# Kernel optimization log

Hardware: AMD Instinct MI355X
Metric: run time of the kernel (lower is better)

## Reference

```python
import jax, jax.numpy as jnp
import numpy as np

B, L_Q, S_KV, H, E = 4, 1024, 1024, 8, 64
IN_CH = OUT_CH = 512
MODES = 64
INDEX_Q = np.arange(MODES)   # 'lowest' mode selection -> range(0, modes)
INDEX_KV = np.arange(MODES)
SCALE = 1.0 / np.sqrt(OUT_CH)
FACTOR = 5


def setup_inputs() -> dict:
    key = jax.random.key(0)
    ks = jax.random.split(key, 7)
    tf_queries = jax.random.normal(ks[0], (B, L_Q, H, E), jnp.float32)
    queries = jax.random.normal(ks[1], (B, L_Q, H, E), jnp.float32)
    keys = jax.random.normal(ks[2], (B, S_KV, H, E), jnp.float32)
    values = jax.random.normal(ks[3], (B, S_KV, H, E), jnp.float32)
    mask = jnp.ones((1,), jnp.int32)  # unused by the module
    weights_fuse = jax.random.uniform(ks[4], (H, L_Q, 2), jnp.float32)
    # torch.rand with cfloat dtype samples re/im independently from U[0,1)
    w1_re = SCALE * jax.random.uniform(ks[5], (H, IN_CH // 8, OUT_CH // 8, MODES), jnp.float32)
    w1_im = SCALE * jax.random.uniform(ks[6], (H, IN_CH // 8, OUT_CH // 8, MODES), jnp.float32)
    return dict(tf_queries=tf_queries, queries=queries, keys=keys, values=values,
                mask=mask, weights_fuse=weights_fuse, w1_re=w1_re, w1_im=w1_im)


def get_sig_scores(n, queries, keys, scale, corr):
    # queries/keys: [B, L, H, E] (keys already aligned to L_Q)
    B_, Lq, H_, E_ = queries.shape
    Lk = keys.shape[1]
    q = jnp.transpose(queries, (0, 2, 1, 3))  # [B,H,L,E]
    k = jnp.transpose(keys, (0, 2, 1, 3))
    if corr:
        qf = jnp.fft.rfft(jnp.transpose(queries, (0, 2, 3, 1)), axis=-1)
        kf = jnp.fft.rfft(jnp.transpose(keys, (0, 2, 3, 1)), axis=-1)
        autocorr = jnp.transpose(jnp.fft.irfft(qf * jnp.conj(kf), axis=-1), (0, 1, 3, 2))  # [B,H,L,E]
    else:
        autocorr = q
    amp = jnp.linalg.norm(autocorr, axis=-1)           # [B,H,L]
    _, top_idx = jax.lax.top_k(amp, n)                 # [B,H,n]
    q_sel = jnp.take_along_axis(q, top_idx[..., None], axis=2)  # [B,H,n,E]
    scores = jnp.einsum('bhnd,bhmd->bhnm', q_sel, k) * scale    # [B,H,n,Lk]
    full = jnp.full((B_, H_, Lq, Lk), -jnp.inf, scores.dtype)
    bi = jnp.arange(B_)[:, None, None]
    hi = jnp.arange(H_)[None, :, None]
    full = full.at[bi, hi, top_idx].set(scores)        # scatter selected query rows
    # softmax over the query axis for every key position (transpose(2,3))
    return jax.nn.softmax(jnp.swapaxes(full, 2, 3), axis=-1)  # [B,H,Lk,Lq]


def reference(tf_queries, queries, keys, values, mask, weights_fuse, w1_re, w1_im):
    B_, Lq, H_, E_ = queries.shape
    S_ = keys.shape[1]
    xq = jnp.transpose(queries, (0, 2, 3, 1))  # [B,H,E,L_Q]
    xk = jnp.transpose(keys, (0, 2, 3, 1))     # [B,H,E,S]
    if Lq > S_:
        pad = jnp.zeros((B_, Lq - S_, H_, E_), keys.dtype)
        keys2 = jnp.concatenate([keys, pad], axis=1)
        values2 = jnp.concatenate([values, pad], axis=1)
    else:
        keys2 = keys[:, :Lq]
        values2 = values[:, :Lq]
    n_top = min(int(FACTOR * np.ceil(np.log(Lq))), Lq)

    attn_t = get_sig_scores(n_top, queries, keys2, SCALE, corr=True)
    attn_tf = get_sig_scores(n_top, tf_queries, keys2, SCALE, corr=False)

    nw = jax.nn.softmax(weights_fuse, axis=-1)  # [H,L_Q,2]
    fused = nw[None, :, :, 0, None] * attn_t + nw[None, :, :, 1, None] * attn_tf
    # dropout(p=0.1) in eval mode -> identity

    xq_ft = jnp.fft.rfft(xq, axis=-1)[:, :, :, INDEX_Q]   # [B,H,E,M]
    xk_ft = jnp.fft.rfft(xk, axis=-1)[:, :, :, INDEX_KV]  # [B,H,E,M]
    xqk = jnp.tanh(jnp.einsum('bhex,bhey->bhxy', xq_ft, xk_ft))  # complex tanh
    xqkv = jnp.einsum('bhxy,bhey->bhex', xqk, xk_ft)
    w1 = w1_re + 1j * w1_im
    xqkvw = jnp.einsum('bhex,heox->bhox', xqkv, w1)        # [B,H,O,M]
    out_ft = jnp.zeros((B_, H_, E_, Lq // 2 + 1), xqkvw.dtype)
    out_ft = out_ft.at[:, :, :, INDEX_Q].set(xqkvw)
    out = jnp.fft.irfft(out_ft / IN_CH / OUT_CH, n=Lq, axis=-1)  # [B,H,E,L_Q]

    output = jnp.einsum('bhlm,bhmd->bhld', fused, jnp.transpose(values2, (0, 2, 1, 3)))
    output = jnp.transpose(output, (0, 1, 3, 2))  # [B,H,D,L_Q]
    return (output + out) * 0.5
```

## Files before the change

kernel.cpp:

```cpp
#include <hip/hip_runtime.h>
#include <math.h>

#define B_ 4
#define H_ 8
#define L_ 1024
#define E_ 64
#define NTOP 35
#define SCALE_ 0.04419417382415922f


__device__ __forceinline__ void dev_stage(char* smem, int vbid,
                                          const float* __restrict__ q_g,
                                          const float* __restrict__ k_g,
                                          float* __restrict__ xtq,
                                          float* __restrict__ xtk) {
  float* tile = reinterpret_cast<float*>(smem);
  const int tc = vbid & 15;
  const int src = (vbid >> 4) & 1;
  const int bh = vbid >> 5;
  const int b = bh >> 3, h = bh & 7;
  const int t0 = tc * 64;
  const int tid = threadIdx.x;
  const float* in = src ? k_g : q_g;
  float* out = src ? xtk : xtq;

  for (int idx = tid; idx < 1024; idx += 256) {
    int t = idx >> 4, e4 = idx & 15;
    float4 v = reinterpret_cast<const float4*>(
        in + ((size_t)(b * L_ + t0 + t) * H_ + h) * E_)[e4];
    tile[t * 65 + e4 * 4 + 0] = v.x; tile[t * 65 + e4 * 4 + 1] = v.y;
    tile[t * 65 + e4 * 4 + 2] = v.z; tile[t * 65 + e4 * 4 + 3] = v.w;
  }
  __syncthreads();
  for (int idx = tid; idx < 1024; idx += 256) {
    int e = idx >> 4, t4 = idx & 15;
    float4 v = make_float4(tile[(t4 * 4 + 0) * 65 + e], tile[(t4 * 4 + 1) * 65 + e],
                           tile[(t4 * 4 + 2) * 65 + e], tile[(t4 * 4 + 3) * 65 + e]);
    reinterpret_cast<float4*>(out + ((size_t)(bh * 64 + e)) * 1024 + t0)[t4] = v;
  }
}

__device__ __forceinline__ void dev_tfqnorm(int vbid,
                                            const float* __restrict__ tfq,
                                            float* __restrict__ ampsum) {
  const int bh = vbid >> 2, qt = vbid & 3;
  const int b = bh >> 3, h = bh & 7;
  const int l = qt * 256 + threadIdx.x;
  const float4* p4 = reinterpret_cast<const float4*>(
      &tfq[((size_t)(b * L_ + l) * H_ + h) * E_]);
  float s = 0.f;
#pragma unroll
  for (int e4 = 0; e4 < 16; ++e4) {
    float4 v = p4[e4];
    s += v.x * v.x + v.y * v.y + v.z * v.z + v.w * v.w;
  }
  ampsum[(size_t)(bh * 2 + 1) * 1024 + l] = s;
}

__device__ __forceinline__ void dev_fft(char* smem, int vbid,
                                        const float* __restrict__ xtq,
                                        const float* __restrict__ xtk,
                                        float* __restrict__ amp2_part,
                                        float* __restrict__ qft,
                                        float* __restrict__ kft) {
  float* zre = reinterpret_cast<float*>(smem);
  float* zim = zre + 4096;
  float* ctab = zim + 4096;
  float* stab = ctab + 512;
  const int eg = vbid & 15;
  const int bh = vbid >> 4;
  const int tid = threadIdx.x;
  const float TWO_PI_N = 6.283185307179586f / 1024.0f;

  if (tid < 512) {
    float s, c;
    sincosf(TWO_PI_N * (float)tid, &s, &c);
    ctab[tid] = c; stab[tid] = s;
  }
  for (int idx = tid; idx < 1024; idx += 512) {
    int ee = idx >> 8, t4 = idx & 255;
    size_t ro = ((size_t)(bh * 64 + eg * 4 + ee)) * 1024;
    float4 qv = reinterpret_cast<const float4*>(xtq + ro)[t4];
    float4 kv = reinterpret_cast<const float4*>(xtk + ro)[t4];
    *reinterpret_cast<float4*>(&zre[ee * 1024 + t4 * 4]) = qv;
    *reinterpret_cast<float4*>(&zim[ee * 1024 + t4 * 4]) = kv;
  }
  __syncthreads();

  for (int s = 0; s < 10; ++s) {
    const int half = 512 >> s;
#pragma unroll
    for (int it = 0; it < 4; ++it) {
      int idx = tid + it * 512;
      int ee = idx >> 9;
      int bf = idx & 511;
      int j = bf & (half - 1);
      int p0 = ((bf >> (9 - s)) << (10 - s)) + j;
      int p1 = p0 + half;
      float ur = zre[ee * 1024 + p0], ui = zim[ee * 1024 + p0];
      float vr = zre[ee * 1024 + p1], vi = zim[ee * 1024 + p1];
      float dr = ur - vr, di = ui - vi;
      zre[ee * 1024 + p0] = ur + vr; zim[ee * 1024 + p0] = ui + vi;
      int twi = j << s;
      float c = ctab[twi], sn = stab[twi];
      zre[ee * 1024 + p1] = fmaf(dr, c, di * sn);
      zim[ee * 1024 + p1] = fmaf(di, c, -dr * sn);
    }
    __syncthreads();
  }

  float pr[8], pi_[8];
#pragma unroll
  for (int it = 0; it < 8; ++it) {
    int idx = tid + it * 512;
    int ee = idx >> 10;
    int p = idx & 1023;
    int m = __brev((unsigned)p) >> 22;
    int mp = (1024 - m) & 1023;
    int pp = __brev((unsigned)mp) >> 22;
    float ar = zre[ee * 1024 + p], ai = zim[ee * 1024 + p];
    float br = zre[ee * 1024 + pp], bi = zim[ee * 1024 + pp];
    float qr = 0.5f * (ar + br), qi = 0.5f * (ai - bi);
    float kr = 0.5f * (ai + bi), ki = -0.5f * (ar - br);
    pr[it]  = fmaf(qr, kr, qi * ki);
    pi_[it] = fmaf(qi, kr, -qr * ki);
    if (m < 64) {
      size_t o = ((size_t)(bh * 64 + eg * 4 + ee) * 64 + m) * 2;
      qft[o] = qr; qft[o + 1] = qi;
      kft[o] = kr; kft[o + 1] = ki;
    }
  }
  __syncthreads();
#pragma unroll
  for (int it = 0; it < 8; ++it) {
    int idx = tid + it * 512;
    int ee = idx >> 10;
    int p = idx & 1023;
    zre[ee * 1024 + p] = pr[it]; zim[ee * 1024 + p] = pi_[it];
  }
  __syncthreads();

  for (int idx = tid; idx < 2048; idx += 512) {
    int u = idx >> 10;
    int p = idx & 1023;
    int e0 = 2 * u, e1 = 2 * u + 1;
    float s_r = zre[e0 * 1024 + p] - zim[e1 * 1024 + p];
    float s_i = zim[e0 * 1024 + p] + zre[e1 * 1024 + p];
    zre[e0 * 1024 + p] = s_r; zim[e0 * 1024 + p] = s_i;
  }
  __syncthreads();

  for (int s = 9; s >= 0; --s) {
    const int half = 512 >> s;
#pragma unroll
    for (int it = 0; it < 2; ++it) {
      int idx = tid + it * 512;
      int ee = (idx >> 9) * 2;
      int bf = idx & 511;
      int j = bf & (half - 1);
      int p0 = ((bf >> (9 - s)) << (10 - s)) + j;
      int p1 = p0 + half;
      int twi = j << s;
      float c = ctab[twi], sn = stab[twi];
      float ur = zre[ee * 1024 + p0], ui = zim[ee * 1024 + p0];
      float wr = zre[ee * 1024 + p1], wi = zim[ee * 1024 + p1];
      float vr = fmaf(wr, c, -wi * sn);
      float vi = fmaf(wi, c, wr * sn);
      zre[ee * 1024 + p0] = ur + vr; zim[ee * 1024 + p0] = ui + vi;
      zre[ee * 1024 + p1] = ur - vr; zim[ee * 1024 + p1] = ui - vi;
    }
    __syncthreads();
  }

  for (int t = tid; t < 1024; t += 512) {
    float r0 = zre[t], i0 = zim[t];
    float r2 = zre[2 * 1024 + t], i2 = zim[2 * 1024 + t];
    amp2_part[(size_t)(bh * 16 + eg) * 1024 + t] =
        fmaf(r0, r0, fmaf(i0, i0, fmaf(r2, r2, i2 * i2)));
  }
}

__device__ __forceinline__ void dev_sel(char* smem, int vbid,
                                        const float* __restrict__ amp2_part,
                                        const float* __restrict__ ampsum,
                                        int* __restrict__ sel_ws) {
  float* amp = reinterpret_cast<float*>(smem);
  const int p = vbid;
  const int tid = threadIdx.x;

  if ((p & 1) == 0) {
    const int bh = p >> 1;
    for (int t = tid; t < 1024; t += 256) {
      float s = 0.f;
#pragma unroll
      for (int c = 0; c < 16; ++c)
        s += amp2_part[(size_t)(bh * 16 + c) * 1024 + t];
      amp[t] = s;
    }
  } else {
    for (int t = tid; t < 1024; t += 256)
      amp[t] = ampsum[(size_t)p * 1024 + t];
  }
  __syncthreads();

  if (tid < 64) {
    const int lane = tid;
    float val[16];
#pragma unroll
    for (int j = 0; j < 16; ++j) val[j] = amp[j * 64 + lane];

    float bv = -1.f; int bi = lane;
#pragma unroll
    for (int j = 0; j < 16; ++j) {
      if (val[j] > bv) { bv = val[j]; bi = j * 64 + lane; }
    }
    for (int it = 0; it < NTOP; ++it) {
      float v = bv; int i = bi;
#pragma unroll
      for (int d = 1; d < 64; d <<= 1) {
        float ov = __shfl_xor(v, d);
        int oi = __shfl_xor(i, d);
        if (ov > v || (ov == v && oi < i)) { v = ov; i = oi; }
      }
      if (lane == 0) sel_ws[p * 64 + it] = i;
      if ((i & 63) == lane) {
        int jr = i >> 6;
#pragma unroll
        for (int j = 0; j < 16; ++j) if (j == jr) val[j] = -1.f;
        bv = -1.f; bi = lane;
#pragma unroll
        for (int j = 0; j < 16; ++j) {
          if (val[j] > bv) { bv = val[j]; bi = j * 64 + lane; }
        }
      }
    }
  }
}

__device__ __forceinline__ void dev_attn(char* smem, int vbid,
                                         const float* __restrict__ q_g,
                                         const float* __restrict__ tfq,
                                         const float* __restrict__ k_g,
                                         const float* __restrict__ v_g,
                                         const float* __restrict__ wfuse,
                                         const int* __restrict__ sel_ws,
                                         float* __restrict__ out) {
  float4* qs4 = reinterpret_cast<float4*>(smem);
  float4* vs4 = qs4 + 2 * NTOP * 16;
  const int ac = vbid & 15;
  const int bh = vbid >> 4;
  const int b = bh >> 3, h = bh & 7;
  const int a0 = ac * 64;
  const int tid = threadIdx.x;

  for (int idx = tid; idx < 2 * NTOP * 16; idx += 256) {
    int src = idx / (NTOP * 16);
    int rem = idx - src * (NTOP * 16);
    int i = rem >> 4, e4 = rem & 15;
    int row = sel_ws[(bh * 2 + src) * 64 + i];
    size_t rb = ((size_t)(b * L_ + row) * H_ + h) * E_;
    const float* qbase = src ? tfq : q_g;
    qs4[(src * NTOP + i) * 16 + e4] = reinterpret_cast<const float4*>(qbase + rb)[e4];
    vs4[(src * NTOP + i) * 16 + e4] = reinterpret_cast<const float4*>(v_g + rb)[e4];
  }
  __syncthreads();

  const int qd = tid & 3, r = tid >> 2;
  const int a = a0 + r;
  const int eb = qd * 16;

  size_t krb = ((size_t)(b * L_ + a) * H_ + h) * E_;
  const float4* k4p = reinterpret_cast<const float4*>(k_g + krb);
  float4 kq[4];
#pragma unroll
  for (int j4 = 0; j4 < 4; ++j4) kq[j4] = k4p[qd * 4 + j4];

  float ct[NTOP], ctf[NTOP];
#pragma unroll
  for (int i = 0; i < NTOP; ++i) { ct[i] = 0.f; ctf[i] = 0.f; }

#pragma unroll
  for (int j4 = 0; j4 < 4; ++j4) {
    float4 kv = kq[j4];
#pragma unroll
    for (int i = 0; i < NTOP; ++i) {
      float4 q4 = qs4[(0 * NTOP + i) * 16 + qd * 4 + j4];
      ct[i] = fmaf(q4.x, kv.x, ct[i]); ct[i] = fmaf(q4.y, kv.y, ct[i]);
      ct[i] = fmaf(q4.z, kv.z, ct[i]); ct[i] = fmaf(q4.w, kv.w, ct[i]);
      float4 p4 = qs4[(1 * NTOP + i) * 16 + qd * 4 + j4];
      ctf[i] = fmaf(p4.x, kv.x, ctf[i]); ctf[i] = fmaf(p4.y, kv.y, ctf[i]);
      ctf[i] = fmaf(p4.z, kv.z, ctf[i]); ctf[i] = fmaf(p4.w, kv.w, ctf[i]);
    }
  }
#pragma unroll
  for (int i = 0; i < NTOP; ++i) {
    ct[i] += __shfl_xor(ct[i], 1);  ct[i] += __shfl_xor(ct[i], 2);
    ctf[i] += __shfl_xor(ctf[i], 1); ctf[i] += __shfl_xor(ctf[i], 2);
  }

  float wf0 = wfuse[(h * L_ + a) * 2 + 0];
  float wf1 = wfuse[(h * L_ + a) * 2 + 1];
  float wm = fmaxf(wf0, wf1);
  float ew0 = expf(wf0 - wm), ew1 = expf(wf1 - wm);
  float nw0 = ew0 / (ew0 + ew1), nw1 = ew1 / (ew0 + ew1);

  {
    float m = -1e30f;
#pragma unroll
    for (int i = 0; i < NTOP; ++i) { ct[i] *= SCALE_; m = fmaxf(m, ct[i]); }
    float sum = 0.f;
#pragma unroll
    for (int i = 0; i < NTOP; ++i) { ct[i] = expf(ct[i] - m); sum += ct[i]; }
    float c = 0.5f * nw0 / sum;
#pragma unroll
    for (int i = 0; i < NTOP; ++i) ct[i] *= c;
  }
  {
    float m = -1e30f;
#pragma unroll
    for (int i = 0; i < NTOP; ++i) { ctf[i] *= SCALE_; m = fmaxf(m, ctf[i]); }
    float sum = 0.f;
#pragma unroll
    for (int i = 0; i < NTOP; ++i) { ctf[i] = expf(ctf[i] - m); sum += ctf[i]; }
    float c = 0.5f * nw1 / sum;
#pragma unroll
    for (int i = 0; i < NTOP; ++i) ctf[i] *= c;
  }
#pragma unroll
  for (int j4 = 0; j4 < 4; ++j4) {
    float ax = 0.f, ay = 0.f, az = 0.f, aw = 0.f;
#pragma unroll
    for (int i = 0; i < NTOP; ++i) {
      float4 v4 = vs4[(0 * NTOP + i) * 16 + qd * 4 + j4];
      ax = fmaf(ct[i], v4.x, ax); ay = fmaf(ct[i], v4.y, ay);
      az = fmaf(ct[i], v4.z, az); aw = fmaf(ct[i], v4.w, aw);
    }
#pragma unroll
    for (int i = 0; i < NTOP; ++i) {
      float4 v4 = vs4[(1 * NTOP + i) * 16 + qd * 4 + j4];
      ax = fmaf(ctf[i], v4.x, ax); ay = fmaf(ctf[i], v4.y, ay);
      az = fmaf(ctf[i], v4.z, az); aw = fmaf(ctf[i], v4.w, aw);
    }
    int d = eb + j4 * 4;
    out[((size_t)(bh * 64 + d + 0)) * 1024 + a] = ax;
    out[((size_t)(bh * 64 + d + 1)) * 1024 + a] = ay;
    out[((size_t)(bh * 64 + d + 2)) * 1024 + a] = az;
    out[((size_t)(bh * 64 + d + 3)) * 1024 + a] = aw;
  }
}

__device__ __forceinline__ void dev_spec12(char* smem, int vbid,
                                           const float* __restrict__ qft,
                                           const float* __restrict__ kft,
                                           float* __restrict__ xre_g,
                                           float* __restrict__ xim_g) {
  float* kre = reinterpret_cast<float*>(smem);
  float* kim = kre + 4160;
  float* qre = kim + 4160;
  float* qim = qre + 512;
  float* tre = qim + 512;
  float* tim = tre + 512;
  const int xc = vbid & 7;
  const int bh = vbid >> 3;
  const int tid = threadIdx.x;

  for (int idx = tid; idx < 4096; idx += 256) {
    int e = idx >> 6, y = idx & 63;
    size_t o = ((size_t)(bh * 64 + e) * 64 + y) * 2;
    kre[e * 65 + y] = kft[o]; kim[e * 65 + y] = kft[o + 1];
  }
  for (int idx = tid; idx < 512; idx += 256) {
    int e = idx >> 3, xl = idx & 7;
    size_t o = ((size_t)(bh * 64 + e) * 64 + xc * 8 + xl) * 2;
    qre[e * 8 + xl] = qft[o]; qim[e * 8 + xl] = qft[o + 1];
  }
  __syncthreads();

  const int y = tid & 63, xg = tid >> 6;
#pragma unroll
  for (int xi = 0; xi < 2; ++xi) {
    int xl = xg + xi * 4;
    float ar = 0.f, ai = 0.f;
    for (int e = 0; e < 64; ++e) {
      float a = qre[e * 8 + xl], b = qim[e * 8 + xl];
      float c = kre[e * 65 + y], d = kim[e * 65 + y];
      ar = fmaf(a, c, fmaf(-b, d, ar));
      ai = fmaf(a, d, fmaf(b, c, ai));
    }
    float trv, tiv;
    float x2 = 2.f * ar, y2 = 2.f * ai;
    if (fabsf(x2) > 30.f) {
      trv = copysignf(1.f, ar); tiv = 0.f;
    } else {
      float sh = sinhf(x2), ch = coshf(x2);
      float sn = sinf(y2), cs = cosf(y2);
      float dd = ch + cs;
      trv = sh / dd; tiv = sn / dd;
    }
    tre[xl * 64 + y] = trv; tim[xl * 64 + y] = tiv;
  }
  __syncthreads();

  const int e2 = tid & 63, xg2 = tid >> 6;
#pragma unroll
  for (int xi = 0; xi < 2; ++xi) {
    int xl = xg2 + xi * 4;
    float ar = 0.f, ai = 0.f;
    for (int yy = 0; yy < 64; ++yy) {
      float a = tre[xl * 64 + yy], b = tim[xl * 64 + yy];
      float c = kre[e2 * 65 + yy], d = kim[e2 * 65 + yy];
      ar = fmaf(a, c, fmaf(-b, d, ar));
      ai = fmaf(a, d, fmaf(b, c, ai));
    }
    xre_g[(size_t)bh * 4096 + (xc * 8 + xl) * 64 + e2] = ar;
    xim_g[(size_t)bh * 4096 + (xc * 8 + xl) * 64 + e2] = ai;
  }
}

__device__ __forceinline__ void dev_w1(char* smem, int vbid,
                                       const float* __restrict__ xre_g,
                                       const float* __restrict__ xim_g,
                                       const float* __restrict__ w1re,
                                       const float* __restrict__ w1im,
                                       float* __restrict__ xw) {
  float* xre = reinterpret_cast<float*>(smem);
  float* xim = xre + 4160;
  float* redr = xim + 4160;
  float* redi = redr + 2048;
  const int oc = vbid & 7;
  const int bh = vbid >> 3;
  const int h = bh & 7;
  const int tid = threadIdx.x;

  for (int idx = tid; idx < 4096; idx += 256) {
    int x = idx >> 6, e = idx & 63;
    xre[e * 65 + x] = xre_g[(size_t)bh * 4096 + idx];
    xim[e * 65 + x] = xim_g[(size_t)bh * 4096 + idx];
  }
  __syncthreads();

  const int x = tid & 63, g = tid >> 6;
  float accr[8], acci[8];
#pragma unroll
  for (int oo = 0; oo < 8; ++oo) { accr[oo] = 0.f; acci[oo] = 0.f; }

  for (int ee = 0; ee < 16; ++ee) {
    int e = g * 16 + ee;
    float a = xre[e * 65 + x], b = xim[e * 65 + x];
    size_t wbase = (((size_t)h * 64 + e) * 64 + oc * 8) * 64 + x;
#pragma unroll
    for (int oo = 0; oo < 8; ++oo) {
      float c = w1re[wbase + (size_t)oo * 64];
      float d = w1im[wbase + (size_t)oo * 64];
      accr[oo] = fmaf(a, c, fmaf(-b, d, accr[oo]));
      acci[oo] = fmaf(a, d, fmaf(b, c, acci[oo]));
    }
  }
#pragma unroll
  for (int oo = 0; oo < 8; ++oo) {
    redr[g * 512 + oo * 64 + x] = accr[oo];
    redi[g * 512 + oo * 64 + x] = acci[oo];
  }
  __syncthreads();

  const float INV = 1.0f / (512.0f * 512.0f);
  for (int idx = tid; idx < 512; idx += 256) {
    int oo = idx >> 6, x2 = idx & 63;
    float r = redr[idx] + redr[512 + idx] + redr[1024 + idx] + redr[1536 + idx];
    float i = redi[idx] + redi[512 + idx] + redi[1024 + idx] + redi[1536 + idx];
    size_t oidx = ((size_t)(bh * 64 + oc * 8 + oo) * 64 + x2) * 2;
    xw[oidx] = r * INV;
    xw[oidx + 1] = i * INV;
  }
}

__device__ __forceinline__ void dev_final(char* smem, int vbid,
                                          const float* __restrict__ xw,
                                          float* __restrict__ out) {
  float* Xre = reinterpret_cast<float*>(smem);
  float* Xim = Xre + 512;
  const int tc = vbid & 3;
  const int oc = (vbid >> 2) & 7;
  const int bh = vbid >> 5;
  const int o0 = oc * 8;
  const int tid = threadIdx.x;

  for (int idx = tid; idx < 512; idx += 256) {
    int o = idx >> 6, m = idx & 63;
    size_t s = ((size_t)(bh * 64 + o0 + o) * 64 + m) * 2;
    Xre[o * 64 + m] = 2.f * xw[s]; Xim[o * 64 + m] = 2.f * xw[s + 1];
  }
  __syncthreads();

  const int t = tc * 256 + tid;
  const float HALF_INVN = 0.5f / 1024.0f;
  const float TWO_PI = 6.283185307179586f;
  float th = TWO_PI * (float)t * (1.0f / 1024.0f);
  float s1, c1;
  __sincosf(th, &s1, &c1);
  float cm = c1, sm = s1;

  float acc[8];
#pragma unroll
  for (int o = 0; o < 8; ++o) acc[o] = 0.5f * Xre[o * 64];

  for (int m = 1; m < 64; ++m) {
#pragma unroll
    for (int o = 0; o < 8; ++o) {
      acc[o] = fmaf(Xre[o * 64 + m], cm, acc[o]);
      acc[o] = fmaf(-Xim[o * 64 + m], sm, acc[o]);
    }
    float cn = fmaf(cm, c1, -sm * s1);
    float sn = fmaf(sm, c1, cm * s1);
    cm = cn; sm = sn;
  }
#pragma unroll
  for (int o = 0; o < 8; ++o) {
    size_t oi = ((size_t)(bh * 64 + o0 + o)) * 1024 + t;
    out[oi] = fmaf(acc[o], HALF_INVN, out[oi]);
  }
}


__global__ __launch_bounds__(256) void k_L1(const float* __restrict__ q,
                                            const float* __restrict__ k,
                                            const float* __restrict__ tfq,
                                            float* __restrict__ xtq,
                                            float* __restrict__ xtk,
                                            float* __restrict__ ampsum) {
  __shared__ __align__(16) char smem[16640];
  if (blockIdx.x < 1024) dev_stage(smem, blockIdx.x, q, k, xtq, xtk);
  else dev_tfqnorm(blockIdx.x - 1024, tfq, ampsum);
}

__global__ __launch_bounds__(512) void k_L2(const float* __restrict__ xtq,
                                            const float* __restrict__ xtk,
                                            float* __restrict__ amp2,
                                            float* __restrict__ qft,
                                            float* __restrict__ kft) {
  __shared__ __align__(16) char smem[36864];
  dev_fft(smem, blockIdx.x, xtq, xtk, amp2, qft, kft);
}

__global__ __launch_bounds__(256) void k_L3(const float* __restrict__ amp2,
                                            const float* __restrict__ ampsum,
                                            int* __restrict__ sel,
                                            const float* __restrict__ qft,
                                            const float* __restrict__ kft,
                                            float* __restrict__ xre_g,
                                            float* __restrict__ xim_g) {
  __shared__ __align__(16) char smem[41472];
  if (blockIdx.x < 64) dev_sel(smem, blockIdx.x, amp2, ampsum, sel);
  else dev_spec12(smem, blockIdx.x - 64, qft, kft, xre_g, xim_g);
}

__global__ __launch_bounds__(256) void k_L4(const float* __restrict__ q,
                                            const float* __restrict__ tfq,
                                            const float* __restrict__ k,
                                            const float* __restrict__ v,
                                            const float* __restrict__ wfuse,
                                            const int* __restrict__ sel,
                                            float* __restrict__ out,
                                            const float* __restrict__ xre_g,
                                            const float* __restrict__ xim_g,
                                            const float* __restrict__ w1re,
                                            const float* __restrict__ w1im,
                                            float* __restrict__ xw) {
  __shared__ __align__(16) char smem[49664];
  if (blockIdx.x < 512) dev_attn(smem, blockIdx.x, q, tfq, k, v, wfuse, sel, out);
  else dev_w1(smem, blockIdx.x - 512, xre_g, xim_g, w1re, w1im, xw);
}

__global__ __launch_bounds__(256) void k_L5(const float* __restrict__ xw,
                                            float* __restrict__ out) {
  __shared__ __align__(16) char smem[4096];
  dev_final(smem, blockIdx.x, xw, out);
}


__global__ __launch_bounds__(256) void k_fft_s(const float* __restrict__ q_g,
                                               const float* __restrict__ k_g,
                                               float* __restrict__ amp2_part,
                                               float* __restrict__ qft,
                                               float* __restrict__ kft) {
  __shared__ float zre[4][1024], zim[4][1024];
  __shared__ float ctab[512], stab[512];
  const int eg = blockIdx.x & 15;
  const int bh = blockIdx.x >> 4;
  const int b = bh >> 3, h = bh & 7;
  const int tid = threadIdx.x;
  const float TWO_PI_N = 6.283185307179586f / 1024.0f;

  for (int j = tid; j < 512; j += 256) {
    float s, c;
    sincosf(TWO_PI_N * (float)j, &s, &c);
    ctab[j] = c; stab[j] = s;
  }
  for (int t = tid; t < 1024; t += 256) {
    size_t g4 = ((size_t)(b * L_ + t) * H_ + h) * 16 + eg;
    float4 qv = reinterpret_cast<const float4*>(q_g)[g4];
    float4 kv = reinterpret_cast<const float4*>(k_g)[g4];
    zre[0][t] = qv.x; zre[1][t] = qv.y; zre[2][t] = qv.z; zre[3][t] = qv.w;
    zim[0][t] = kv.x; zim[1][t] = kv.y; zim[2][t] = kv.z; zim[3][t] = kv.w;
  }
  __syncthreads();

  for (int s = 0; s < 10; ++s) {
    const int half = 512 >> s;
#pragma unroll
    for (int it = 0; it < 8; ++it) {
      int idx = tid + it * 256;
      int ee = idx >> 9;
      int bf = idx & 511;
      int j = bf & (half - 1);
      int p0 = ((bf >> (9 - s)) << (10 - s)) + j;
      int p1 = p0 + half;
      float ur = zre[ee][p0], ui = zim[ee][p0];
      float vr = zre[ee][p1], vi = zim[ee][p1];
      float dr = ur - vr, di = ui - vi;
      zre[ee][p0] = ur + vr; zim[ee][p0] = ui + vi;
      int twi = j << s;
      float c = ctab[twi], sn = stab[twi];
      zre[ee][p1] = fmaf(dr, c, di * sn);
      zim[ee][p1] = fmaf(di, c, -dr * sn);
    }
    __syncthreads();
  }

  float pr[16], pi_[16];
#pragma unroll
  for (int it = 0; it < 16; ++it) {
    int idx = tid + it * 256;
    int ee = idx >> 10;
    int p = idx & 1023;
    int m = __brev((unsigned)p) >> 22;
    int mp = (1024 - m) & 1023;
    int pp = __brev((unsigned)mp) >> 22;
    float ar = zre[ee][p], ai = zim[ee][p];
    float br = zre[ee][pp], bi = zim[ee][pp];
    float qr = 0.5f * (ar + br), qi = 0.5f * (ai - bi);
    float kr = 0.5f * (ai + bi), ki = -0.5f * (ar - br);
    pr[it]  = fmaf(qr, kr, qi * ki);
    pi_[it] = fmaf(qi, kr, -qr * ki);
    if (m < 64) {
      size_t o = ((size_t)(bh * 64 + eg * 4 + ee) * 64 + m) * 2;
      qft[o] = qr; qft[o + 1] = qi;
      kft[o] = kr; kft[o + 1] = ki;
    }
  }
  __syncthreads();
#pragma unroll
  for (int it = 0; it < 16; ++it) {
    int idx = tid + it * 256;
    int ee = idx >> 10;
    int p = idx & 1023;
    zre[ee][p] = pr[it]; zim[ee][p] = pi_[it];
  }
  __syncthreads();

  for (int idx = tid; idx < 2048; idx += 256) {
    int u = idx >> 10;
    int p = idx & 1023;
    int e0 = 2 * u, e1 = 2 * u + 1;
    float s_r = zre[e0][p] - zim[e1][p];
    float s_i = zim[e0][p] + zre[e1][p];
    zre[e0][p] = s_r; zim[e0][p] = s_i;
  }
  __syncthreads();

  for (int s = 9; s >= 0; --s) {
    const int half = 512 >> s;
#pragma unroll
    for (int it = 0; it < 4; ++it) {
      int idx = tid + it * 256;
      int ee = (idx >> 9) * 2;
      int bf = idx & 511;
      int j = bf & (half - 1);
      int p0 = ((bf >> (9 - s)) << (10 - s)) + j;
      int p1 = p0 + half;
      int twi = j << s;
      float c = ctab[twi], sn = stab[twi];
      float ur = zre[ee][p0], ui = zim[ee][p0];
      float wr = zre[ee][p1], wi = zim[ee][p1];
      float vr = fmaf(wr, c, -wi * sn);
      float vi = fmaf(wi, c, wr * sn);
      zre[ee][p0] = ur + vr; zim[ee][p0] = ui + vi;
      zre[ee][p1] = ur - vr; zim[ee][p1] = ui - vi;
    }
    __syncthreads();
  }

  for (int t = tid; t < 1024; t += 256) {
    float r0 = zre[0][t], i0 = zim[0][t];
    float r2 = zre[2][t], i2 = zim[2][t];
    amp2_part[(size_t)(bh * 16 + eg) * 1024 + t] =
        fmaf(r0, r0, fmaf(i0, i0, fmaf(r2, r2, i2 * i2)));
  }
}

__global__ __launch_bounds__(256) void k_topk(const float* __restrict__ amp2_part,
                                              const float* __restrict__ tfq,
                                              int* __restrict__ sel_ws) {
  __shared__ float amp[1024];
  __shared__ float wv_s[4];
  __shared__ int wi_s[4];
  __shared__ int winner_s;
  const int src = blockIdx.x & 1;
  const int bh = blockIdx.x >> 1;
  const int b = bh >> 3, h = bh & 7;
  const int tid = threadIdx.x;

  if (src == 0) {
    for (int t = tid; t < 1024; t += 256) {
      float s = 0.f;
#pragma unroll
      for (int c = 0; c < 16; ++c) s += amp2_part[(size_t)(bh * 16 + c) * 1024 + t];
      amp[t] = s;
    }
  } else {
    for (int l = tid; l < 1024; l += 256) {
      const float4* p4 = reinterpret_cast<const float4*>(
          &tfq[((size_t)(b * L_ + l) * H_ + h) * E_]);
      float s = 0.f;
#pragma unroll
      for (int e4 = 0; e4 < 16; ++e4) {
        float4 v = p4[e4];
        s += v.x * v.x + v.y * v.y + v.z * v.z + v.w * v.w;
      }
      amp[l] = s;
    }
  }
  __syncthreads();

  float bv = -1.f; int bi = tid;
#pragma unroll
  for (int kk = 0; kk < 4; ++kk) {
    int t = tid + kk * 256;
    float v = amp[t];
    if (v > bv) { bv = v; bi = t; }
  }
  const int lane = tid & 63, w = tid >> 6;

  for (int it = 0; it < NTOP; ++it) {
    float v = bv; int i = bi;
#pragma unroll
    for (int d = 1; d < 64; d <<= 1) {
      float ov = __shfl_xor(v, d);
      int oi = __shfl_xor(i, d);
      if (ov > v || (ov == v && oi < i)) { v = ov; i = oi; }
    }
    if (lane == 0) { wv_s[w] = v; wi_s[w] = i; }
    __syncthreads();
    if (tid == 0) {
      float fv = wv_s[0]; int fi = wi_s[0];
#pragma unroll
      for (int j = 1; j < 4; ++j) {
        if (wv_s[j] > fv || (wv_s[j] == fv && wi_s[j] < fi)) { fv = wv_s[j]; fi = wi_s[j]; }
      }
      winner_s = fi;
      sel_ws[(bh * 2 + src) * 64 + it] = fi;
    }
    __syncthreads();
    int fi = winner_s;
    if ((fi & 255) == tid) {
      amp[fi] = -1.f;
      bv = -1.f; bi = tid;
#pragma unroll
      for (int kk = 0; kk < 4; ++kk) {
        int t = tid + kk * 256;
        float vv = amp[t];
        if (vv > bv) { bv = vv; bi = t; }
      }
    }
  }
}

__global__ __launch_bounds__(256) void k_attn_w(const float* __restrict__ q,
                                                const float* __restrict__ tfq,
                                                const float* __restrict__ k,
                                                const float* __restrict__ v,
                                                const float* __restrict__ wfuse,
                                                const int* __restrict__ sel,
                                                float* __restrict__ out) {
  __shared__ __align__(16) char smem[35840];
  dev_attn(smem, blockIdx.x, q, tfq, k, v, wfuse, sel, out);
}

__global__ __launch_bounds__(256) void k_spec12_w(const float* __restrict__ qft,
                                                  const float* __restrict__ kft,
                                                  float* __restrict__ xre_g,
                                                  float* __restrict__ xim_g) {
  __shared__ __align__(16) char smem[41472];
  dev_spec12(smem, blockIdx.x, qft, kft, xre_g, xim_g);
}

__global__ __launch_bounds__(256) void k_w1_w(const float* __restrict__ xre_g,
                                              const float* __restrict__ xim_g,
                                              const float* __restrict__ w1re,
                                              const float* __restrict__ w1im,
                                              float* __restrict__ xw) {
  __shared__ __align__(16) char smem[49664];
  dev_w1(smem, blockIdx.x, xre_g, xim_g, w1re, w1im, xw);
}

extern "C" void kernel_launch(void* const* d_in, const int* in_sizes, int n_in,
                              void* d_out, int out_size, void* d_ws, size_t ws_size,
                              hipStream_t stream) {
  const float* tfq   = (const float*)d_in[0];
  const float* q     = (const float*)d_in[1];
  const float* k     = (const float*)d_in[2];
  const float* v     = (const float*)d_in[3];
  const float* wfuse = (const float*)d_in[5];
  const float* w1re  = (const float*)d_in[6];
  const float* w1im  = (const float*)d_in[7];
  float* out = (float*)d_out;
  float* ws  = (float*)d_ws;

  const size_t STAGED_FLOATS = 5312512;
  if (ws_size >= STAGED_FLOATS * sizeof(float)) {
    float* xtq    = ws;
    float* xtk    = ws + 2097152;
    float* amp2   = ws + 4194304;
    float* qft    = ws + 4718592;
    float* kft    = ws + 4980736;
    int*   sel    = (int*)(ws + 5242880);
    float* ampsum = ws + 5246976;
    float* xre_g  = ws;
    float* xim_g  = ws + 131072;
    float* xw     = ws + 262144;

    k_L1<<<1152, 256, 0, stream>>>(q, k, tfq, xtq, xtk, ampsum);
    k_L2<<<512, 512, 0, stream>>>(xtq, xtk, amp2, qft, kft);
    k_L3<<<320, 256, 0, stream>>>(amp2, ampsum, sel, qft, kft, xre_g, xim_g);
    k_L4<<<768, 256, 0, stream>>>(q, tfq, k, v, wfuse, sel, out,
                                  xre_g, xim_g, w1re, w1im, xw);
    k_L5<<<1024, 256, 0, stream>>>(xw, out);
  } else {
    float* amp2  = ws;
    float* xre_g = ws;
    float* xim_g = ws + 131072;
    float* xw    = ws + 262144;
    float* qft   = ws + 524288;
    float* kft   = ws + 786432;
    int*   sel   = (int*)(ws + 1048576);

    k_fft_s<<<512, 256, 0, stream>>>(q, k, amp2, qft, kft);
    k_topk<<<64, 256, 0, stream>>>(amp2, tfq, sel);
    k_attn_w<<<512, 256, 0, stream>>>(q, tfq, k, v, wfuse, sel, out);
    k_spec12_w<<<256, 256, 0, stream>>>(qft, kft, xre_g, xim_g);
    k_w1_w<<<256, 256, 0, stream>>>(xre_g, xim_g, w1re, w1im, xw);
    k_L5<<<1024, 256, 0, stream>>>(xw, out);
  }
}
```

Before: 114.0 us.

## Fuse W1 mixing with the inverse-DFT epilogue and accumulate into output with atomics

Adds a W1 stage that performs the complex W1 mixing and then evaluates the truncated inverse real DFT directly, using a sincos twiddle recurrence over the 64 modes. Its result is atomically added into the output. The attention blocks also switch to atomic adds, and the output is zeroed with a memset at the start. This removes the separate final kernel and the xw intermediate round trip through global memory. In exchange it adds a memset, atomic traffic to every output element, and recurrence-based twiddles that may accumulate rounding error.

```diff
diff --git a/kernel.cpp b/kernel.cpp
--- a/kernel.cpp
+++ b/kernel.cpp
@@ -342,10 +342,10 @@
       az = fmaf(ctf[i], v4.z, az); aw = fmaf(ctf[i], v4.w, aw);
     }
     int d = eb + j4 * 4;
-    out[((size_t)(bh * 64 + d + 0)) * 1024 + a] = ax;
-    out[((size_t)(bh * 64 + d + 1)) * 1024 + a] = ay;
-    out[((size_t)(bh * 64 + d + 2)) * 1024 + a] = az;
-    out[((size_t)(bh * 64 + d + 3)) * 1024 + a] = aw;
+    atomicAdd(&out[((size_t)(bh * 64 + d + 0)) * 1024 + a], ax);
+    atomicAdd(&out[((size_t)(bh * 64 + d + 1)) * 1024 + a], ay);
+    atomicAdd(&out[((size_t)(bh * 64 + d + 2)) * 1024 + a], az);
+    atomicAdd(&out[((size_t)(bh * 64 + d + 3)) * 1024 + a], aw);
   }
 }
 
@@ -417,6 +417,102 @@
   }
 }
 
+__device__ __forceinline__ void dev_w1final(char* smem, int vbid,
+                                            const float* __restrict__ xre_g,
+                                            const float* __restrict__ xim_g,
+                                            const float* __restrict__ w1re,
+                                            const float* __restrict__ w1im,
+                                            float* __restrict__ out) {
+  float* xre = reinterpret_cast<float*>(smem);
+  float* xim = xre + 4160;
+  float* redr = xim + 4160;
+  float* redi = redr + 2048;
+  float* Xre = xre;
+  float* Xim = xre + 512;
+  const int oc = vbid & 7;
+  const int bh = vbid >> 3;
+  const int h = bh & 7;
+  const int o0 = oc * 8;
+  const int tid = threadIdx.x;
+
+  for (int idx = tid; idx < 4096; idx += 256) {
+    int x = idx >> 6, e = idx & 63;
+    xre[e * 65 + x] = xre_g[(size_t)bh * 4096 + idx];
+    xim[e * 65 + x] = xim_g[(size_t)bh * 4096 + idx];
+  }
+  __syncthreads();
+
+  const int x = tid & 63, g = tid >> 6;
+  float accr[8], acci[8];
+#pragma unroll
+  for (int oo = 0; oo < 8; ++oo) { accr[oo] = 0.f; acci[oo] = 0.f; }
+
+  for (int ee = 0; ee < 16; ++ee) {
+    int e = g * 16 + ee;
+    float a = xre[e * 65 + x], b = xim[e * 65 + x];
+    size_t wbase = (((size_t)h * 64 + e) * 64 + o0) * 64 + x;
+#pragma unroll
+    for (int oo = 0; oo < 8; ++oo) {
+      float c = w1re[wbase + (size_t)oo * 64];
+      float d = w1im[wbase + (size_t)oo * 64];
+      accr[oo] = fmaf(a, c, fmaf(-b, d, accr[oo]));
+      acci[oo] = fmaf(a, d, fmaf(b, c, acci[oo]));
+    }
+  }
+#pragma unroll
+  for (int oo = 0; oo < 8; ++oo) {
+    redr[g * 512 + oo * 64 + x] = accr[oo];
+    redi[g * 512 + oo * 64 + x] = acci[oo];
+  }
+  __syncthreads();
+
+  const float INV = 1.0f / (512.0f * 512.0f);
+  float xv[2][2];
+#pragma unroll
+  for (int it = 0; it < 2; ++it) {
+    int idx = tid + it * 256;
+    float r = redr[idx] + redr[512 + idx] + redr[1024 + idx] + redr[1536 + idx];
+    float i = redi[idx] + redi[512 + idx] + redi[1024 + idx] + redi[1536 + idx];
+    xv[it][0] = 2.f * (r * INV);
+    xv[it][1] = 2.f * (i * INV);
+  }
+  __syncthreads();
+#pragma unroll
+  for (int it = 0; it < 2; ++it) {
+    int idx = tid + it * 256;
+    Xre[idx] = xv[it][0];
+    Xim[idx] = xv[it][1];
+  }
+  __syncthreads();
+
+  const float HALF_INVN = 0.5f / 1024.0f;
+  const float TWO_PI = 6.283185307179586f;
+  for (int tc = 0; tc < 4; ++tc) {
+    int t = tc * 256 + tid;
+    float th = TWO_PI * (float)t * (1.0f / 1024.0f);
+    float s1, c1;
+    __sincosf(th, &s1, &c1);
+    float cm = c1, sm = s1;
+    float acc[8];
+#pragma unroll
+    for (int o = 0; o < 8; ++o) acc[o] = 0.5f * Xre[o * 64];
+    for (int m = 1; m < 64; ++m) {
+#pragma unroll
+      for (int o = 0; o < 8; ++o) {
+        acc[o] = fmaf(Xre[o * 64 + m], cm, acc[o]);
+        acc[o] = fmaf(-Xim[o * 64 + m], sm, acc[o]);
+      }
+      float cn = fmaf(cm, c1, -sm * s1);
+      float sn = fmaf(sm, c1, cm * s1);
+      cm = cn; sm = sn;
+    }
+#pragma unroll
+    for (int o = 0; o < 8; ++o) {
+      atomicAdd(&out[((size_t)(bh * 64 + o0 + o)) * 1024 + t], acc[o] * HALF_INVN);
+    }
+  }
+}
+
 __device__ __forceinline__ void dev_w1(char* smem, int vbid,
                                        const float* __restrict__ xre_g,
                                        const float* __restrict__ xim_g,
@@ -554,21 +650,20 @@
   else dev_spec12(smem, blockIdx.x - 64, qft, kft, xre_g, xim_g);
 }
 
-__global__ __launch_bounds__(256) void k_L4(const float* __restrict__ q,
-                                            const float* __restrict__ tfq,
-                                            const float* __restrict__ k,
-                                            const float* __restrict__ v,
-                                            const float* __restrict__ wfuse,
-                                            const int* __restrict__ sel,
-                                            float* __restrict__ out,
-                                            const float* __restrict__ xre_g,
-                                            const float* __restrict__ xim_g,
-                                            const float* __restrict__ w1re,
-                                            const float* __restrict__ w1im,
-                                            float* __restrict__ xw) {
+__global__ __launch_bounds__(256) void k_L4f(const float* __restrict__ q,
+                                             const float* __restrict__ tfq,
+                                             const float* __restrict__ k,
+                                             const float* __restrict__ v,
+                                             const float* __restrict__ wfuse,
+                                             const int* __restrict__ sel,
+                                             float* __restrict__ out,
+                                             const float* __restrict__ xre_g,
+                                             const float* __restrict__ xim_g,
+                                             const float* __restrict__ w1re,
+                                             const float* __restrict__ w1im) {
   __shared__ __align__(16) char smem[49664];
   if (blockIdx.x < 512) dev_attn(smem, blockIdx.x, q, tfq, k, v, wfuse, sel, out);
-  else dev_w1(smem, blockIdx.x - 512, xre_g, xim_g, w1re, w1im, xw);
+  else dev_w1final(smem, blockIdx.x - 512, xre_g, xim_g, w1re, w1im, out);
 }
 
 __global__ __launch_bounds__(256) void k_L5(const float* __restrict__ xw,
@@ -816,6 +911,8 @@
   float* out = (float*)d_out;
   float* ws  = (float*)d_ws;
 
+  hipMemsetAsync(out, 0, (size_t)out_size * sizeof(float), stream);
+
   const size_t STAGED_FLOATS = 5312512;
   if (ws_size >= STAGED_FLOATS * sizeof(float)) {
     float* xtq    = ws;
@@ -827,14 +924,12 @@
     float* ampsum = ws + 5246976;
     float* xre_g  = ws;
     float* xim_g  = ws + 131072;
-    float* xw     = ws + 262144;
 
     k_L1<<<1152, 256, 0, stream>>>(q, k, tfq, xtq, xtk, ampsum);
     k_L2<<<512, 512, 0, stream>>>(xtq, xtk, amp2, qft, kft);
     k_L3<<<320, 256, 0, stream>>>(amp2, ampsum, sel, qft, kft, xre_g, xim_g);
-    k_L4<<<768, 256, 0, stream>>>(q, tfq, k, v, wfuse, sel, out,
-                                  xre_g, xim_g, w1re, w1im, xw);
-    k_L5<<<1024, 256, 0, stream>>>(xw, out);
+    k_L4f<<<768, 256, 0, stream>>>(q, tfq, k, v, wfuse, sel, out,
+                                   xre_g, xim_g, w1re, w1im);
   } else {
     float* amp2  = ws;
     float* xre_g = ws;
```

After: 120.5 us. +5.6%, slower.

## Process two key rows per thread in attention, restructure w1 complex GEMM

Applied to the files above, without the earlier changes.

The attention kernel now makes each block cover 128 key positions instead of 64, with every thread handling two rows. This reuses the gathered top-k query and value rows staged in shared memory across twice the work and halves the number of blocks that reload them. The w1 stage drops its split-E partial sums and shared-memory reduction, so each thread loops over all 64 E values for two outputs. That shrinks shared memory, but it quadruples the serial loop length and doubles the register count in attention, which risks spills and lower occupancy.

```diff
diff --git a/kernel.cpp b/kernel.cpp
--- a/kernel.cpp
+++ b/kernel.cpp
@@ -237,20 +237,20 @@
   }
 }
 
-__device__ __forceinline__ void dev_attn(char* smem, int vbid,
-                                         const float* __restrict__ q_g,
-                                         const float* __restrict__ tfq,
-                                         const float* __restrict__ k_g,
-                                         const float* __restrict__ v_g,
-                                         const float* __restrict__ wfuse,
-                                         const int* __restrict__ sel_ws,
-                                         float* __restrict__ out) {
+__device__ __forceinline__ void dev_attn2(char* smem, int vbid,
+                                          const float* __restrict__ q_g,
+                                          const float* __restrict__ tfq,
+                                          const float* __restrict__ k_g,
+                                          const float* __restrict__ v_g,
+                                          const float* __restrict__ wfuse,
+                                          const int* __restrict__ sel_ws,
+                                          float* __restrict__ out) {
   float4* qs4 = reinterpret_cast<float4*>(smem);
   float4* vs4 = qs4 + 2 * NTOP * 16;
-  const int ac = vbid & 15;
-  const int bh = vbid >> 4;
+  const int ac = vbid & 7;
+  const int bh = vbid >> 3;
   const int b = bh >> 3, h = bh & 7;
-  const int a0 = ac * 64;
+  const int a0 = ac * 128;
   const int tid = threadIdx.x;
 
   for (int idx = tid; idx < 2 * NTOP * 16; idx += 256) {
@@ -266,86 +266,126 @@
   __syncthreads();
 
   const int qd = tid & 3, r = tid >> 2;
-  const int a = a0 + r;
+  const int aA = a0 + r, aB = a0 + 64 + r;
   const int eb = qd * 16;
 
-  size_t krb = ((size_t)(b * L_ + a) * H_ + h) * E_;
-  const float4* k4p = reinterpret_cast<const float4*>(k_g + krb);
-  float4 kq[4];
-#pragma unroll
-  for (int j4 = 0; j4 < 4; ++j4) kq[j4] = k4p[qd * 4 + j4];
-
-  float ct[NTOP], ctf[NTOP];
-#pragma unroll
-  for (int i = 0; i < NTOP; ++i) { ct[i] = 0.f; ctf[i] = 0.f; }
+  size_t krbA = ((size_t)(b * L_ + aA) * H_ + h) * E_;
+  size_t krbB = ((size_t)(b * L_ + aB) * H_ + h) * E_;
+  const float4* kA = reinterpret_cast<const float4*>(k_g + krbA);
+  const float4* kB = reinterpret_cast<const float4*>(k_g + krbB);
+  float4 kqA[4], kqB[4];
+#pragma unroll
+  for (int j4 = 0; j4 < 4; ++j4) { kqA[j4] = kA[qd * 4 + j4]; kqB[j4] = kB[qd * 4 + j4]; }
+
+  float ctA[NTOP], ctfA[NTOP], ctB[NTOP], ctfB[NTOP];
+#pragma unroll
+  for (int i = 0; i < NTOP; ++i) { ctA[i] = 0.f; ctfA[i] = 0.f; ctB[i] = 0.f; ctfB[i] = 0.f; }
 
 #pragma unroll
   for (int j4 = 0; j4 < 4; ++j4) {
-    float4 kv = kq[j4];
+    float4 kvA = kqA[j4], kvB = kqB[j4];
 #pragma unroll
     for (int i = 0; i < NTOP; ++i) {
       float4 q4 = qs4[(0 * NTOP + i) * 16 + qd * 4 + j4];
-      ct[i] = fmaf(q4.x, kv.x, ct[i]); ct[i] = fmaf(q4.y, kv.y, ct[i]);
-      ct[i] = fmaf(q4.z, kv.z, ct[i]); ct[i] = fmaf(q4.w, kv.w, ct[i]);
+      ctA[i] = fmaf(q4.x, kvA.x, ctA[i]); ctA[i] = fmaf(q4.y, kvA.y, ctA[i]);
+      ctA[i] = fmaf(q4.z, kvA.z, ctA[i]); ctA[i] = fmaf(q4.w, kvA.w, ctA[i]);
+      ctB[i] = fmaf(q4.x, kvB.x, ctB[i]); ctB[i] = fmaf(q4.y, kvB.y, ctB[i]);
+      ctB[i] = fmaf(q4.z, kvB.z, ctB[i]); ctB[i] = fmaf(q4.w, kvB.w, ctB[i]);
       float4 p4 = qs4[(1 * NTOP + i) * 16 + qd * 4 + j4];
-      ctf[i] = fmaf(p4.x, kv.x, ctf[i]); ctf[i] = fmaf(p4.y, kv.y, ctf[i]);
-      ctf[i] = fmaf(p4.z, kv.z, ctf[i]); ctf[i] = fmaf(p4.w, kv.w, ctf[i]);
+      ctfA[i] = fmaf(p4.x, kvA.x, ctfA[i]); ctfA[i] = fmaf(p4.y, kvA.y, ctfA[i]);
+      ctfA[i] = fmaf(p4.z, kvA.z, ctfA[i]); ctfA[i] = fmaf(p4.w, kvA.w, ctfA[i]);
+      ctfB[i] = fmaf(p4.x, kvB.x, ctfB[i]); ctfB[i] = fmaf(p4.y, kvB.y, ctfB[i]);
+      ctfB[i] = fmaf(p4.z, kvB.z, ctfB[i]); ctfB[i] = fmaf(p4.w, kvB.w, ctfB[i]);
     }
   }
 #pragma unroll
   for (int i = 0; i < NTOP; ++i) {
-    ct[i] += __shfl_xor(ct[i], 1);  ct[i] += __shfl_xor(ct[i], 2);
-    ctf[i] += __shfl_xor(ctf[i], 1); ctf[i] += __shfl_xor(ctf[i], 2);
-  }
-
-  float wf0 = wfuse[(h * L_ + a) * 2 + 0];
-  float wf1 = wfuse[(h * L_ + a) * 2 + 1];
-  float wm = fmaxf(wf0, wf1);
-  float ew0 = expf(wf0 - wm), ew1 = expf(wf1 - wm);
-  float nw0 = ew0 / (ew0 + ew1), nw1 = ew1 / (ew0 + ew1);
+    ctA[i] += __shfl_xor(ctA[i], 1);  ctA[i] += __shfl_xor(ctA[i], 2);
+    ctfA[i] += __shfl_xor(ctfA[i], 1); ctfA[i] += __shfl_xor(ctfA[i], 2);
+    ctB[i] += __shfl_xor(ctB[i], 1);  ctB[i] += __shfl_xor(ctB[i], 2);
+    ctfB[i] += __shfl_xor(ctfB[i], 1); ctfB[i] += __shfl_xor(ctfB[i], 2);
+  }
 
   {
+    float wf0 = wfuse[(h * L_ + aA) * 2 + 0];
+    float wf1 = wfuse[(h * L_ + aA) * 2 + 1];
+    float wm = fmaxf(wf0, wf1);
+    float ew0 = expf(wf0 - wm), ew1 = expf(wf1 - wm);
+    float nw0 = ew0 / (ew0 + ew1), nw1 = ew1 / (ew0 + ew1);
     float m = -1e30f;
 #pragma unroll
-    for (int i = 0; i < NTOP; ++i) { ct[i] *= SCALE_; m = fmaxf(m, ct[i]); }
+    for (int i = 0; i < NTOP; ++i) { ctA[i] *= SCALE_; m = fmaxf(m, ctA[i]); }
     float sum = 0.f;
 #pragma unroll
-    for (int i = 0; i < NTOP; ++i) { ct[i] = expf(ct[i] - m); sum += ct[i]; }
+    for (int i = 0; i < NTOP; ++i) { ctA[i] = expf(ctA[i] - m); sum += ctA[i]; }
     float c = 0.5f * nw0 / sum;
 #pragma unroll
-    for (int i = 0; i < NTOP; ++i) ct[i] *= c;
+    for (int i = 0; i < NTOP; ++i) ctA[i] *= c;
+    float m2 = -1e30f;
+#pragma unroll
+    for (int i = 0; i < NTOP; ++i) { ctfA[i] *= SCALE_; m2 = fmaxf(m2, ctfA[i]); }
+    float sum2 = 0.f;
+#pragma unroll
+    for (int i = 0; i < NTOP; ++i) { ctfA[i] = expf(ctfA[i] - m2); sum2 += ctfA[i]; }
+    float c2 = 0.5f * nw1 / sum2;
+#pragma unroll
+    for (int i = 0; i < NTOP; ++i) ctfA[i] *= c2;
   }
   {
+    float wf0 = wfuse[(h * L_ + aB) * 2 + 0];
+    float wf1 = wfuse[(h * L_ + aB) * 2 + 1];
+    float wm = fmaxf(wf0, wf1);
+    float ew0 = expf(wf0 - wm), ew1 = expf(wf1 - wm);
+    float nw0 = ew0 / (ew0 + ew1), nw1 = ew1 / (ew0 + ew1);
     float m = -1e30f;
 #pragma unroll
-    for (int i = 0; i < NTOP; ++i) { ctf[i] *= SCALE_; m = fmaxf(m, ctf[i]); }
+    for (int i = 0; i < NTOP; ++i) { ctB[i] *= SCALE_; m = fmaxf(m, ctB[i]); }
     float sum = 0.f;
 #pragma unroll
-    for (int i = 0; i < NTOP; ++i) { ctf[i] = expf(ctf[i] - m); sum += ctf[i]; }
-    float c = 0.5f * nw1 / sum;
-#pragma unroll
-    for (int i = 0; i < NTOP; ++i) ctf[i] *= c;
-  }
+    for (int i = 0; i < NTOP; ++i) { ctB[i] = expf(ctB[i] - m); sum += ctB[i]; }
+    float c = 0.5f * nw0 / sum;
+#pragma unroll
+    for (int i = 0; i < NTOP; ++i) ctB[i] *= c;
+    float m2 = -1e30f;
+#pragma unroll
+    for (int i = 0; i < NTOP; ++i) { ctfB[i] *= SCALE_; m2 = fmaxf(m2, ctfB[i]); }
+    float sum2 = 0.f;
+#pragma unroll
+    for (int i = 0; i < NTOP; ++i) { ctfB[i] = expf(ctfB[i] - m2); sum2 += ctfB[i]; }
+    float c2 = 0.5f * nw1 / sum2;
+#pragma unroll
+    for (int i = 0; i < NTOP; ++i) ctfB[i] *= c2;
+  }
+
 #pragma unroll
   for (int j4 = 0; j4 < 4; ++j4) {
-    float ax = 0.f, ay = 0.f, az = 0.f, aw = 0.f;
+    float axA = 0.f, ayA = 0.f, azA = 0.f, awA = 0.f;
+    float axB = 0.f, ayB = 0.f, azB = 0.f, awB = 0.f;
 #pragma unroll
     for (int i = 0; i < NTOP; ++i) {
       float4 v4 = vs4[(0 * NTOP + i) * 16 + qd * 4 + j4];
-      ax = fmaf(ct[i], v4.x, ax); ay = fmaf(ct[i], v4.y, ay);
-      az = fmaf(ct[i], v4.z, az); aw = fmaf(ct[i], v4.w, aw);
+      axA = fmaf(ctA[i], v4.x, axA); ayA = fmaf(ctA[i], v4.y, ayA);
+      azA = fmaf(ctA[i], v4.z, azA); awA = fmaf(ctA[i], v4.w, awA);
+      axB = fmaf(ctB[i], v4.x, axB); ayB = fmaf(ctB[i], v4.y, ayB);
+      azB = fmaf(ctB[i], v4.z, azB); awB = fmaf(ctB[i], v4.w, awB);
     }
 #pragma unroll
     for (int i = 0; i < NTOP; ++i) {
       float4 v4 = vs4[(1 * NTOP + i) * 16 + qd * 4 + j4];
-      ax = fmaf(ctf[i], v4.x, ax); ay = fmaf(ctf[i], v4.y, ay);
-      az = fmaf(ctf[i], v4.z, az); aw = fmaf(ctf[i], v4.w, aw);
+      axA = fmaf(ctfA[i], v4.x, axA); ayA = fmaf(ctfA[i], v4.y, ayA);
+      azA = fmaf(ctfA[i], v4.z, azA); awA = fmaf(ctfA[i], v4.w, awA);
+      axB = fmaf(ctfB[i], v4.x, axB); ayB = fmaf(ctfB[i], v4.y, ayB);
+      azB = fmaf(ctfB[i], v4.z, azB); awB = fmaf(ctfB[i], v4.w, awB);
     }
     int d = eb + j4 * 4;
-    out[((size_t)(bh * 64 + d + 0)) * 1024 + a] = ax;
-    out[((size_t)(bh * 64 + d + 1)) * 1024 + a] = ay;
-    out[((size_t)(bh * 64 + d + 2)) * 1024 + a] = az;
-    out[((size_t)(bh * 64 + d + 3)) * 1024 + a] = aw;
+    out[((size_t)(bh * 64 + d + 0)) * 1024 + aA] = axA;
+    out[((size_t)(bh * 64 + d + 1)) * 1024 + aA] = ayA;
+    out[((size_t)(bh * 64 + d + 2)) * 1024 + aA] = azA;
+    out[((size_t)(bh * 64 + d + 3)) * 1024 + aA] = awA;
+    out[((size_t)(bh * 64 + d + 0)) * 1024 + aB] = axB;
+    out[((size_t)(bh * 64 + d + 1)) * 1024 + aB] = ayB;
+    out[((size_t)(bh * 64 + d + 2)) * 1024 + aB] = azB;
+    out[((size_t)(bh * 64 + d + 3)) * 1024 + aB] = awB;
   }
 }
 
@@ -425,8 +465,6 @@
                                        float* __restrict__ xw) {
   float* xre = reinterpret_cast<float*>(smem);
   float* xim = xre + 4160;
-  float* redr = xim + 4160;
-  float* redi = redr + 2048;
   const int oc = vbid & 7;
   const int bh = vbid >> 3;
   const int h = bh & 7;
@@ -440,38 +478,23 @@
   __syncthreads();
 
   const int x = tid & 63, g = tid >> 6;
-  float accr[8], acci[8];
-#pragma unroll
-  for (int oo = 0; oo < 8; ++oo) { accr[oo] = 0.f; acci[oo] = 0.f; }
-
-  for (int ee = 0; ee < 16; ++ee) {
-    int e = g * 16 + ee;
+  const int o0 = oc * 8 + g * 2;
+  float ar0 = 0.f, ai0 = 0.f, ar1 = 0.f, ai1 = 0.f;
+  for (int e = 0; e < 64; ++e) {
     float a = xre[e * 65 + x], b = xim[e * 65 + x];
-    size_t wbase = (((size_t)h * 64 + e) * 64 + oc * 8) * 64 + x;
-#pragma unroll
-    for (int oo = 0; oo < 8; ++oo) {
-      float c = w1re[wbase + (size_t)oo * 64];
-      float d = w1im[wbase + (size_t)oo * 64];
-      accr[oo] = fmaf(a, c, fmaf(-b, d, accr[oo]));
-      acci[oo] = fmaf(a, d, fmaf(b, c, acci[oo]));
-    }
-  }
-#pragma unroll
-  for (int oo = 0; oo < 8; ++oo) {
-    redr[g * 512 + oo * 64 + x] = accr[oo];
-    redi[g * 512 + oo * 64 + x] = acci[oo];
-  }
-  __syncthreads();
-
+    size_t wb = (((size_t)h * 64 + e) * 64 + o0) * 64 + x;
+    float c0 = w1re[wb], d0 = w1im[wb];
+    float c1 = w1re[wb + 64], d1 = w1im[wb + 64];
+    ar0 = fmaf(a, c0, fmaf(-b, d0, ar0));
+    ai0 = fmaf(a, d0, fmaf(b, c0, ai0));
+    ar1 = fmaf(a, c1, fmaf(-b, d1, ar1));
+    ai1 = fmaf(a, d1, fmaf(b, c1, ai1));
+  }
   const float INV = 1.0f / (512.0f * 512.0f);
-  for (int idx = tid; idx < 512; idx += 256) {
-    int oo = idx >> 6, x2 = idx & 63;
-    float r = redr[idx] + redr[512 + idx] + redr[1024 + idx] + redr[1536 + idx];
-    float i = redi[idx] + redi[512 + idx] + redi[1024 + idx] + redi[1536 + idx];
-    size_t oidx = ((size_t)(bh * 64 + oc * 8 + oo) * 64 + x2) * 2;
-    xw[oidx] = r * INV;
-    xw[oidx + 1] = i * INV;
-  }
+  size_t oidx0 = ((size_t)(bh * 64 + o0) * 64 + x) * 2;
+  xw[oidx0] = ar0 * INV; xw[oidx0 + 1] = ai0 * INV;
+  size_t oidx1 = ((size_t)(bh * 64 + o0 + 1) * 64 + x) * 2;
+  xw[oidx1] = ar1 * INV; xw[oidx1 + 1] = ai1 * INV;
 }
 
 __device__ __forceinline__ void dev_final(char* smem, int vbid,
@@ -566,9 +589,9 @@
                                             const float* __restrict__ w1re,
                                             const float* __restrict__ w1im,
                                             float* __restrict__ xw) {
-  __shared__ __align__(16) char smem[49664];
-  if (blockIdx.x < 512) dev_attn(smem, blockIdx.x, q, tfq, k, v, wfuse, sel, out);
-  else dev_w1(smem, blockIdx.x - 512, xre_g, xim_g, w1re, w1im, xw);
+  __shared__ __align__(16) char smem[35840];
+  if (blockIdx.x < 256) dev_attn2(smem, blockIdx.x, q, tfq, k, v, wfuse, sel, out);
+  else dev_w1(smem, blockIdx.x - 256, xre_g, xim_g, w1re, w1im, xw);
 }
 
 __global__ __launch_bounds__(256) void k_L5(const float* __restrict__ xw,
@@ -783,7 +806,7 @@
                                                 const int* __restrict__ sel,
                                                 float* __restrict__ out) {
   __shared__ __align__(16) char smem[35840];
-  dev_attn(smem, blockIdx.x, q, tfq, k, v, wfuse, sel, out);
+  dev_attn2(smem, blockIdx.x, q, tfq, k, v, wfuse, sel, out);
 }
 
 __global__ __launch_bounds__(256) void k_spec12_w(const float* __restrict__ qft,
@@ -799,7 +822,7 @@
                                               const float* __restrict__ w1re,
                                               const float* __restrict__ w1im,
                                               float* __restrict__ xw) {
-  __shared__ __align__(16) char smem[49664];
+  __shared__ __align__(16) char smem[33280];
   dev_w1(smem, blockIdx.x, xre_g, xim_g, w1re, w1im, xw);
 }
 
@@ -832,7 +855,7 @@
     k_L1<<<1152, 256, 0, stream>>>(q, k, tfq, xtq, xtk, ampsum);
     k_L2<<<512, 512, 0, stream>>>(xtq, xtk, amp2, qft, kft);
     k_L3<<<320, 256, 0, stream>>>(amp2, ampsum, sel, qft, kft, xre_g, xim_g);
-    k_L4<<<768, 256, 0, stream>>>(q, tfq, k, v, wfuse, sel, out,
+    k_L4<<<512, 256, 0, stream>>>(q, tfq, k, v, wfuse, sel, out,
                                   xre_g, xim_g, w1re, w1im, xw);
     k_L5<<<1024, 256, 0, stream>>>(xw, out);
   } else {
@@ -846,7 +869,7 @@
 
     k_fft_s<<<512, 256, 0, stream>>>(q, k, amp2, qft, kft);
     k_topk<<<64, 256, 0, stream>>>(amp2, tfq, sel);
-    k_attn_w<<<512, 256, 0, stream>>>(q, tfq, k, v, wfuse, sel, out);
+    k_attn_w<<<256, 256, 0, stream>>>(q, tfq, k, v, wfuse, sel, out);
     k_spec12_w<<<256, 256, 0, stream>>>(qft, kft, xre_g, xim_g);
     k_w1_w<<<256, 256, 0, stream>>>(xre_g, xim_g, w1re, w1im, xw);
     k_L5<<<1024, 256, 0, stream>>>(xw, out);
```

New measurement: 128.8 us. 13.0% more time.
